# Kernel tuning notes

Measured on AMD Instinct MI355X. Metric: run time of the kernel, lower is better.

The kernel has to match this reference:

```python
import jax, jax.numpy as jnp
import numpy as np
from jax import lax

B, DIN, DOUT, DEPTH = 4096, 2048, 2048, 16


def setup_inputs() -> dict:
    key = jax.random.key(0)
    k1, k2, k3, k4 = jax.random.split(key, 4)
    return {
        "x": jax.random.normal(k1, (B, DIN), jnp.float32),
        "absolute_weights": jax.random.normal(k2, (DEPTH, DIN, DOUT), jnp.float32),
        "classical_weights": jax.random.normal(k3, (DIN, DOUT), jnp.float32),
        "classical_biases": jax.random.normal(k4, (DOUT,), jnp.float32),
    }


def _absolute_probs(W):
    # W: [depth, din, dout]; the torch code indexes W[d, j, g] with j over
    # output dims and g in {0,1,2} (3 gates per depth step).
    din = W.shape[1]
    dout = DOUT
    # angles per output j, flattened over (depth, gate): [dout, depth*3]
    ang = jnp.transpose(W[:, :dout, :3], (1, 0, 2)).reshape(dout, -1)
    s0 = jnp.ones((din,), W.dtype) / np.float32(np.sqrt(din))

    def step(s, a):
        # The dense "rotation" matrix built in torch is: diag=cos,
        # superdiag (wrapped) = -sin, subdiag (wrapped) = +sin, i.e.
        # (M s)[i] = cos*s[i] - sin*s[(i+1)%n] + sin*s[(i-1)%n].
        c, si = jnp.cos(a), jnp.sin(a)
        s_new = c * s - si * jnp.roll(s, -1) + si * jnp.roll(s, 1)
        return s_new, None

    def per_j(angs):
        s, _ = lax.scan(step, s0, angs)
        return jnp.abs(s[0]) ** 2

    return jax.vmap(per_j)(ang)  # [dout]


def reference(x, absolute_weights, classical_weights, classical_biases):
    classical = x @ classical_weights + classical_biases  # [B, dout]
    probs = _absolute_probs(absolute_weights)             # [dout], batch-independent
    return jnp.tanh(classical + probs[None, :])
```

## Files before the change

kernel.cpp:

```cpp
#include <hip/hip_runtime.h>
#include <math.h>

#define BATCH 4096
#define DIN   2048
#define DOUT  2048
#define DEPTH 16

typedef unsigned short u16;
typedef __attribute__((ext_vector_type(8))) short short8;
typedef __attribute__((ext_vector_type(4))) float f32x4;


__device__ static inline unsigned bf16_rn(float x) {
    unsigned u = __float_as_uint(x);
    return (u + 0x7FFFu + ((u >> 16) & 1u)) >> 16;
}

__device__ static inline float tanh_fast(float z) {
    float zc = fminf(fmaxf(z, -15.0f), 15.0f);
    float e = __builtin_amdgcn_exp2f(zc * 2.8853900817779268f);
    return (e - 1.0f) * __builtin_amdgcn_rcpf(e + 1.0f);
}

__device__ static inline void async16(u16* lds, const u16* g) {
    __builtin_amdgcn_global_load_lds(
        (const __attribute__((address_space(1))) void*)g,
        (__attribute__((address_space(3))) void*)lds, 16, 0, 0);
}

__global__ __launch_bounds__(256) void probs_kernel(const float* __restrict__ W,
                                                    float* __restrict__ probs) {
    int tid = threadIdx.x;
    int jl = tid >> 4, d = tid & 15;
    int j = blockIdx.x * 16 + jl;
    const float* p = W + (size_t)d * DIN * DOUT + (size_t)j * DOUT;
    float pr = cosf(p[0]) * cosf(p[1]) * cosf(p[2]);
#pragma unroll
    for (int off = 1; off < 16; off <<= 1) pr *= __shfl_xor(pr, off, 16);
    if (d == 0) probs[j] = pr * pr * (1.0f / (float)DIN);
}

__global__ __launch_bounds__(256) void convert_x_kernel(const float* __restrict__ x,
                                                        u16* __restrict__ xh,
                                                        u16* __restrict__ xl) {
    int i = (blockIdx.x * 256 + threadIdx.x) * 4;
    float4 v = *(const float4*)(x + i);
    ushort4 h, l;
    float vv[4] = {v.x, v.y, v.z, v.w};
    u16 hh[4], ll[4];
#pragma unroll
    for (int c = 0; c < 4; ++c) {
        unsigned hb = bf16_rn(vv[c]);
        hh[c] = (u16)hb;
        float r = vv[c] - __uint_as_float(hb << 16);
        ll[c] = (u16)bf16_rn(r);
    }
    h.x = hh[0]; h.y = hh[1]; h.z = hh[2]; h.w = hh[3];
    l.x = ll[0]; l.y = ll[1]; l.z = ll[2]; l.w = ll[3];
    *(ushort4*)(xh + i) = h;
    *(ushort4*)(xl + i) = l;
}

__global__ __launch_bounds__(256) void transpose_w_kernel(const float* __restrict__ W,
                                                          u16* __restrict__ wh,
                                                          u16* __restrict__ wl) {
    __shared__ float t[32][33];
    int n0 = blockIdx.x * 32, k0 = blockIdx.y * 32;
    int tx = threadIdx.x & 31, ty = threadIdx.x >> 5;
#pragma unroll
    for (int i = 0; i < 4; ++i)
        t[ty + i * 8][tx] = W[(size_t)(k0 + ty + i * 8) * DOUT + n0 + tx];
    __syncthreads();
#pragma unroll
    for (int i = 0; i < 4; ++i) {
        float v = t[tx][ty + i * 8];
        size_t o = (size_t)(n0 + ty + i * 8) * DIN + k0 + tx;
        unsigned hb = bf16_rn(v);
        wh[o] = (u16)hb;
        float r = v - __uint_as_float(hb << 16);
        wl[o] = (u16)bf16_rn(r);
    }
}

__global__ __launch_bounds__(256, 2) void gemm_mfma_kernel(
    const u16* __restrict__ xh, const u16* __restrict__ xl,
    const u16* __restrict__ wh, const u16* __restrict__ wl,
    const float* __restrict__ bias, const float* __restrict__ probs,
    float* __restrict__ C)
{
    __shared__ u16 sAh[4096];
    __shared__ u16 sAl[4096];
    __shared__ u16 sBh[4096];
    __shared__ u16 sBl[4096];

    const int tid = threadIdx.x;
    const int lane = tid & 63;
    const int wave = tid >> 6;
    const int bR = blockIdx.y * 128;
    const int bC = blockIdx.x * 128;

    const u16* gsrc = (wave == 0) ? xh + (size_t)bR * DIN
                    : (wave == 1) ? xl + (size_t)bR * DIN
                    : (wave == 2) ? wh + (size_t)bC * DIN
                                  : wl + (size_t)bC * DIN;
    u16* lbase = (wave == 0) ? sAh : (wave == 1) ? sAl : (wave == 2) ? sBh : sBl;

    int goff[8];
#pragma unroll
    for (int i = 0; i < 8; ++i) {
        int row = i * 16 + (lane >> 2);
        int lq = (lane & 3) ^ ((row >> 1) & 3);
        goff[i] = row * DIN + lq * 8;
    }

    const int wm = wave >> 1, wn = wave & 1;
    const int colL = lane & 15, quad = lane >> 4;

    int aoff[4], boff[4];
#pragma unroll
    for (int mt = 0; mt < 4; ++mt) {
        int r = wm * 64 + mt * 16 + colL;
        aoff[mt] = r * 32 + (quad ^ ((r >> 1) & 3)) * 8;
    }
#pragma unroll
    for (int nt = 0; nt < 4; ++nt) {
        int r = wn * 64 + nt * 16 + colL;
        boff[nt] = r * 32 + (quad ^ ((r >> 1) & 3)) * 8;
    }

    f32x4 acc[4][4];
#pragma unroll
    for (int mt = 0; mt < 4; ++mt)
#pragma unroll
        for (int nt = 0; nt < 4; ++nt) acc[mt][nt] = (f32x4){0.f, 0.f, 0.f, 0.f};

    for (int k0 = 0; k0 < DIN; k0 += 32) {
        __syncthreads();
#pragma unroll
        for (int i = 0; i < 8; ++i)
            async16(lbase + i * 512, gsrc + goff[i] + k0);
        __syncthreads();

        short8 ah[4], al[4], bh[4], bl[4];
#pragma unroll
        for (int mt = 0; mt < 4; ++mt) {
            ah[mt] = *(const short8*)&sAh[aoff[mt]];
            al[mt] = *(const short8*)&sAl[aoff[mt]];
        }
#pragma unroll
        for (int nt = 0; nt < 4; ++nt) {
            bh[nt] = *(const short8*)&sBh[boff[nt]];
            bl[nt] = *(const short8*)&sBl[boff[nt]];
        }

#pragma unroll
        for (int mt = 0; mt < 4; ++mt)
#pragma unroll
            for (int nt = 0; nt < 4; ++nt) {
                acc[mt][nt] = __builtin_amdgcn_mfma_f32_16x16x32_bf16(
                    ah[mt], bh[nt], acc[mt][nt], 0, 0, 0);
                acc[mt][nt] = __builtin_amdgcn_mfma_f32_16x16x32_bf16(
                    ah[mt], bl[nt], acc[mt][nt], 0, 0, 0);
                acc[mt][nt] = __builtin_amdgcn_mfma_f32_16x16x32_bf16(
                    al[mt], bh[nt], acc[mt][nt], 0, 0, 0);
            }
    }

    float bp[4];
#pragma unroll
    for (int nt = 0; nt < 4; ++nt) {
        int c = bC + wn * 64 + nt * 16 + colL;
        bp[nt] = bias[c] + probs[c];
    }
#pragma unroll
    for (int mt = 0; mt < 4; ++mt)
#pragma unroll
        for (int nt = 0; nt < 4; ++nt) {
            int c = bC + wn * 64 + nt * 16 + colL;
#pragma unroll
            for (int reg = 0; reg < 4; ++reg) {
                int r = bR + wm * 64 + mt * 16 + quad * 4 + reg;
                C[(size_t)r * DOUT + c] = tanh_fast(acc[mt][nt][reg] + bp[nt]);
            }
        }
}

__global__ __launch_bounds__(256) void gemm_tanh_kernel(
    const float* __restrict__ A, const float* __restrict__ Bw,
    const float* __restrict__ bias, const float* __restrict__ probs,
    float* __restrict__ C)
{
    __shared__ float As[16][128 + 4];
    __shared__ float Bs[16][128 + 4];
    const int tid = threadIdx.x;
    const int block_row = blockIdx.y * 128;
    const int block_col = blockIdx.x * 128;
    const int tr = (tid >> 4) << 3;
    const int tc = (tid & 15) << 3;
    const int a_row = tid >> 2;
    const int a_col = (tid & 3) << 2;
    const int b_row = tid >> 5;
    const int b_col = (tid & 31) << 2;
    const float* Aptr0 = A + (size_t)(block_row + a_row) * DIN + a_col;
    const float* Aptr1 = Aptr0 + (size_t)64 * DIN;
    const float* Bptr0 = Bw + (size_t)b_row * DOUT + block_col + b_col;
    const float* Bptr1 = Bptr0 + (size_t)8 * DOUT;
    float acc[8][8] = {};
    for (int k0 = 0; k0 < DIN; k0 += 16) {
        float4 a0 = *(const float4*)(Aptr0 + k0);
        float4 a1 = *(const float4*)(Aptr1 + k0);
        float4 b0 = *(const float4*)(Bptr0 + (size_t)k0 * DOUT);
        float4 b1 = *(const float4*)(Bptr1 + (size_t)k0 * DOUT);
        __syncthreads();
        As[a_col + 0][a_row] = a0.x;
        As[a_col + 1][a_row] = a0.y;
        As[a_col + 2][a_row] = a0.z;
        As[a_col + 3][a_row] = a0.w;
        As[a_col + 0][a_row + 64] = a1.x;
        As[a_col + 1][a_row + 64] = a1.y;
        As[a_col + 2][a_row + 64] = a1.z;
        As[a_col + 3][a_row + 64] = a1.w;
        *(float4*)&Bs[b_row][b_col]     = b0;
        *(float4*)&Bs[b_row + 8][b_col] = b1;
        __syncthreads();
#pragma unroll
        for (int kk = 0; kk < 16; ++kk) {
            float ar[8], br[8];
#pragma unroll
            for (int i = 0; i < 8; ++i) ar[i] = As[kk][tr + i];
#pragma unroll
            for (int i = 0; i < 8; ++i) br[i] = Bs[kk][tc + i];
#pragma unroll
            for (int i = 0; i < 8; ++i)
#pragma unroll
                for (int jj = 0; jj < 8; ++jj)
                    acc[i][jj] = fmaf(ar[i], br[jj], acc[i][jj]);
        }
    }
    float bp[8];
#pragma unroll
    for (int jj = 0; jj < 8; ++jj)
        bp[jj] = bias[block_col + tc + jj] + probs[block_col + tc + jj];
#pragma unroll
    for (int i = 0; i < 8; ++i) {
        float* crow = C + (size_t)(block_row + tr + i) * DOUT + block_col + tc;
#pragma unroll
        for (int jj = 0; jj < 8; ++jj)
            crow[jj] = tanh_fast(acc[i][jj] + bp[jj]);
    }
}

extern "C" void kernel_launch(void* const* d_in, const int* in_sizes, int n_in,
                              void* d_out, int out_size, void* d_ws, size_t ws_size,
                              hipStream_t stream) {
    const float* x  = (const float*)d_in[0];
    const float* W  = (const float*)d_in[1];
    const float* cw = (const float*)d_in[2];
    const float* cb = (const float*)d_in[3];
    float* out = (float*)d_out;

    const size_t PROBS_B = 8192;
    const size_t XSZ = (size_t)BATCH * DIN;
    const size_t WSZ = (size_t)DIN * DOUT;
    const size_t need = PROBS_B + 2 * XSZ * 2 + 2 * WSZ * 2;

    float* probs = (float*)d_ws;
    probs_kernel<<<DOUT / 16, 256, 0, stream>>>(W, probs);

    if (ws_size >= need) {
        u16* xh = (u16*)((char*)d_ws + PROBS_B);
        u16* xl = xh + XSZ;
        u16* wh = xl + XSZ;
        u16* wl = wh + WSZ;

        convert_x_kernel<<<XSZ / 4 / 256, 256, 0, stream>>>(x, xh, xl);
        transpose_w_kernel<<<dim3(DOUT / 32, DIN / 32), 256, 0, stream>>>(cw, wh, wl);

        dim3 grid(DOUT / 128, BATCH / 128);
        gemm_mfma_kernel<<<grid, 256, 0, stream>>>(xh, xl, wh, wl, cb, probs, out);
    } else {
        dim3 grid(DOUT / 128, BATCH / 128);
        gemm_tanh_kernel<<<grid, 256, 0, stream>>>(x, cw, cb, probs, out);
    }
}
```

Baseline: 432.6 us.

## Fuse preprocessing, probs and MFMA GEMM into one cooperative kernel with grid sync

Merges the probs, x split-conversion, weight transpose/split and MFMA GEMM kernels into a single cooperative launch of 512 blocks. Each block does a slice of the preprocessing, then all blocks meet at a grid-wide barrier before running the GEMM tile. The bias is folded into the probs vector ahead of time. This removes three kernel launches and the gaps between them, at the cost of a grid sync and a dependence on all 512 blocks being co-resident. It also drops the fp32 fallback path, so it needs enough workspace.

```diff
diff --git a/kernel.cpp b/kernel.cpp
--- a/kernel.cpp
+++ b/kernel.cpp
@@ -1,5 +1,8 @@
 #include <hip/hip_runtime.h>
+#include <hip/hip_cooperative_groups.h>
 #include <math.h>
+
+namespace cg = cooperative_groups;
 
 #define BATCH 4096
 #define DIN   2048
@@ -28,76 +31,87 @@
         (__attribute__((address_space(3))) void*)lds, 16, 0, 0);
 }
 
-__global__ __launch_bounds__(256) void probs_kernel(const float* __restrict__ W,
-                                                    float* __restrict__ probs) {
-    int tid = threadIdx.x;
-    int jl = tid >> 4, d = tid & 15;
-    int j = blockIdx.x * 16 + jl;
-    const float* p = W + (size_t)d * DIN * DOUT + (size_t)j * DOUT;
-    float pr = cosf(p[0]) * cosf(p[1]) * cosf(p[2]);
-#pragma unroll
-    for (int off = 1; off < 16; off <<= 1) pr *= __shfl_xor(pr, off, 16);
-    if (d == 0) probs[j] = pr * pr * (1.0f / (float)DIN);
-}
-
-__global__ __launch_bounds__(256) void convert_x_kernel(const float* __restrict__ x,
-                                                        u16* __restrict__ xh,
-                                                        u16* __restrict__ xl) {
-    int i = (blockIdx.x * 256 + threadIdx.x) * 4;
-    float4 v = *(const float4*)(x + i);
-    ushort4 h, l;
-    float vv[4] = {v.x, v.y, v.z, v.w};
-    u16 hh[4], ll[4];
-#pragma unroll
-    for (int c = 0; c < 4; ++c) {
-        unsigned hb = bf16_rn(vv[c]);
-        hh[c] = (u16)hb;
-        float r = vv[c] - __uint_as_float(hb << 16);
-        ll[c] = (u16)bf16_rn(r);
-    }
-    h.x = hh[0]; h.y = hh[1]; h.z = hh[2]; h.w = hh[3];
-    l.x = ll[0]; l.y = ll[1]; l.z = ll[2]; l.w = ll[3];
-    *(ushort4*)(xh + i) = h;
-    *(ushort4*)(xl + i) = l;
-}
-
-__global__ __launch_bounds__(256) void transpose_w_kernel(const float* __restrict__ W,
-                                                          u16* __restrict__ wh,
-                                                          u16* __restrict__ wl) {
-    __shared__ float t[32][33];
-    int n0 = blockIdx.x * 32, k0 = blockIdx.y * 32;
-    int tx = threadIdx.x & 31, ty = threadIdx.x >> 5;
-#pragma unroll
-    for (int i = 0; i < 4; ++i)
-        t[ty + i * 8][tx] = W[(size_t)(k0 + ty + i * 8) * DOUT + n0 + tx];
-    __syncthreads();
-#pragma unroll
-    for (int i = 0; i < 4; ++i) {
-        float v = t[tx][ty + i * 8];
-        size_t o = (size_t)(n0 + ty + i * 8) * DIN + k0 + tx;
-        unsigned hb = bf16_rn(v);
-        wh[o] = (u16)hb;
-        float r = v - __uint_as_float(hb << 16);
-        wl[o] = (u16)bf16_rn(r);
-    }
-}
-
-__global__ __launch_bounds__(256, 2) void gemm_mfma_kernel(
-    const u16* __restrict__ xh, const u16* __restrict__ xl,
-    const u16* __restrict__ wh, const u16* __restrict__ wl,
-    const float* __restrict__ bias, const float* __restrict__ probs,
+__global__ __launch_bounds__(256, 2) void fused_kernel(
+    const float* __restrict__ x,
+    const float* __restrict__ W,
+    const float* __restrict__ cw,
+    const float* __restrict__ cb,
+    u16* __restrict__ xh, u16* __restrict__ xl,
+    u16* __restrict__ wh, u16* __restrict__ wl,
+    float* __restrict__ bp,
     float* __restrict__ C)
 {
-    __shared__ u16 sAh[4096];
-    __shared__ u16 sAl[4096];
-    __shared__ u16 sBh[4096];
-    __shared__ u16 sBl[4096];
-
+    __shared__ u16 smem[16384];
     const int tid = threadIdx.x;
+    const int bid = blockIdx.x;
+
+#pragma unroll
+    for (int g = 0; g < 16; ++g) {
+        int i = (bid * 4096 + g * 256 + tid) * 4;
+        float4 v = *(const float4*)(x + i);
+        float vv[4] = {v.x, v.y, v.z, v.w};
+        u16 hh[4], ll[4];
+#pragma unroll
+        for (int c = 0; c < 4; ++c) {
+            unsigned hb = bf16_rn(vv[c]);
+            hh[c] = (u16)hb;
+            float r = vv[c] - __uint_as_float(hb << 16);
+            ll[c] = (u16)bf16_rn(r);
+        }
+        ushort4 h, l;
+        h.x = hh[0]; h.y = hh[1]; h.z = hh[2]; h.w = hh[3];
+        l.x = ll[0]; l.y = ll[1]; l.z = ll[2]; l.w = ll[3];
+        *(ushort4*)(xh + i) = h;
+        *(ushort4*)(xl + i) = l;
+    }
+
+    {
+        float* t = (float*)smem;
+        const int tx = tid & 31, ty = tid >> 5;
+#pragma unroll
+        for (int it = 0; it < 8; ++it) {
+            int tile = bid * 8 + it;
+            int n0 = (tile & 63) * 32;
+            int k0 = (tile >> 6) * 32;
+            __syncthreads();
+#pragma unroll
+            for (int r = 0; r < 4; ++r)
+                t[(ty + r * 8) * 33 + tx] =
+                    cw[(size_t)(k0 + ty + r * 8) * DOUT + n0 + tx];
+            __syncthreads();
+#pragma unroll
+            for (int r = 0; r < 4; ++r) {
+                float v = t[tx * 33 + ty + r * 8];
+                size_t o = (size_t)(n0 + ty + r * 8) * DIN + k0 + tx;
+                unsigned hb = bf16_rn(v);
+                wh[o] = (u16)hb;
+                float rr = v - __uint_as_float(hb << 16);
+                wl[o] = (u16)bf16_rn(rr);
+            }
+        }
+    }
+
+    if (bid < 128) {
+        int jl = tid >> 4, d = tid & 15;
+        int j = bid * 16 + jl;
+        const float* p = W + (size_t)d * DIN * DOUT + (size_t)j * DOUT;
+        float pr = cosf(p[0]) * cosf(p[1]) * cosf(p[2]);
+#pragma unroll
+        for (int off = 1; off < 16; off <<= 1) pr *= __shfl_xor(pr, off, 16);
+        if (d == 0) bp[j] = pr * pr * (1.0f / (float)DIN) + cb[j];
+    }
+
+    cg::this_grid().sync();
+
+    u16* sAh = smem;
+    u16* sAl = smem + 4096;
+    u16* sBh = smem + 8192;
+    u16* sBl = smem + 12288;
+
     const int lane = tid & 63;
     const int wave = tid >> 6;
-    const int bR = blockIdx.y * 128;
-    const int bC = blockIdx.x * 128;
+    const int bC = (bid & 15) * 128;
+    const int bR = (bid >> 4) * 128;
 
     const u16* gsrc = (wave == 0) ? xh + (size_t)bR * DIN
                     : (wave == 1) ? xl + (size_t)bR * DIN
@@ -166,12 +180,10 @@
             }
     }
 
-    float bp[4];
-#pragma unroll
-    for (int nt = 0; nt < 4; ++nt) {
-        int c = bC + wn * 64 + nt * 16 + colL;
-        bp[nt] = bias[c] + probs[c];
-    }
+    float bpv[4];
+#pragma unroll
+    for (int nt = 0; nt < 4; ++nt)
+        bpv[nt] = bp[bC + wn * 64 + nt * 16 + colL];
 #pragma unroll
     for (int mt = 0; mt < 4; ++mt)
 #pragma unroll
@@ -180,74 +192,9 @@
 #pragma unroll
             for (int reg = 0; reg < 4; ++reg) {
                 int r = bR + wm * 64 + mt * 16 + quad * 4 + reg;
-                C[(size_t)r * DOUT + c] = tanh_fast(acc[mt][nt][reg] + bp[nt]);
+                C[(size_t)r * DOUT + c] = tanh_fast(acc[mt][nt][reg] + bpv[nt]);
             }
         }
-}
-
-__global__ __launch_bounds__(256) void gemm_tanh_kernel(
-    const float* __restrict__ A, const float* __restrict__ Bw,
-    const float* __restrict__ bias, const float* __restrict__ probs,
-    float* __restrict__ C)
-{
-    __shared__ float As[16][128 + 4];
-    __shared__ float Bs[16][128 + 4];
-    const int tid = threadIdx.x;
-    const int block_row = blockIdx.y * 128;
-    const int block_col = blockIdx.x * 128;
-    const int tr = (tid >> 4) << 3;
-    const int tc = (tid & 15) << 3;
-    const int a_row = tid >> 2;
-    const int a_col = (tid & 3) << 2;
-    const int b_row = tid >> 5;
-    const int b_col = (tid & 31) << 2;
-    const float* Aptr0 = A + (size_t)(block_row + a_row) * DIN + a_col;
-    const float* Aptr1 = Aptr0 + (size_t)64 * DIN;
-    const float* Bptr0 = Bw + (size_t)b_row * DOUT + block_col + b_col;
-    const float* Bptr1 = Bptr0 + (size_t)8 * DOUT;
-    float acc[8][8] = {};
-    for (int k0 = 0; k0 < DIN; k0 += 16) {
-        float4 a0 = *(const float4*)(Aptr0 + k0);
-        float4 a1 = *(const float4*)(Aptr1 + k0);
-        float4 b0 = *(const float4*)(Bptr0 + (size_t)k0 * DOUT);
-        float4 b1 = *(const float4*)(Bptr1 + (size_t)k0 * DOUT);
-        __syncthreads();
-        As[a_col + 0][a_row] = a0.x;
-        As[a_col + 1][a_row] = a0.y;
-        As[a_col + 2][a_row] = a0.z;
-        As[a_col + 3][a_row] = a0.w;
-        As[a_col + 0][a_row + 64] = a1.x;
-        As[a_col + 1][a_row + 64] = a1.y;
-        As[a_col + 2][a_row + 64] = a1.z;
-        As[a_col + 3][a_row + 64] = a1.w;
-        *(float4*)&Bs[b_row][b_col]     = b0;
-        *(float4*)&Bs[b_row + 8][b_col] = b1;
-        __syncthreads();
-#pragma unroll
-        for (int kk = 0; kk < 16; ++kk) {
-            float ar[8], br[8];
-#pragma unroll
-            for (int i = 0; i < 8; ++i) ar[i] = As[kk][tr + i];
-#pragma unroll
-            for (int i = 0; i < 8; ++i) br[i] = Bs[kk][tc + i];
-#pragma unroll
-            for (int i = 0; i < 8; ++i)
-#pragma unroll
-                for (int jj = 0; jj < 8; ++jj)
-                    acc[i][jj] = fmaf(ar[i], br[jj], acc[i][jj]);
-        }
-    }
-    float bp[8];
-#pragma unroll
-    for (int jj = 0; jj < 8; ++jj)
-        bp[jj] = bias[block_col + tc + jj] + probs[block_col + tc + jj];
-#pragma unroll
-    for (int i = 0; i < 8; ++i) {
-        float* crow = C + (size_t)(block_row + tr + i) * DOUT + block_col + tc;
-#pragma unroll
-        for (int jj = 0; jj < 8; ++jj)
-            crow[jj] = tanh_fast(acc[i][jj] + bp[jj]);
-    }
 }
 
 extern "C" void kernel_launch(void* const* d_in, const int* in_sizes, int n_in,
@@ -262,24 +209,16 @@
     const size_t PROBS_B = 8192;
     const size_t XSZ = (size_t)BATCH * DIN;
     const size_t WSZ = (size_t)DIN * DOUT;
-    const size_t need = PROBS_B + 2 * XSZ * 2 + 2 * WSZ * 2;
-
-    float* probs = (float*)d_ws;
-    probs_kernel<<<DOUT / 16, 256, 0, stream>>>(W, probs);
-
-    if (ws_size >= need) {
-        u16* xh = (u16*)((char*)d_ws + PROBS_B);
-        u16* xl = xh + XSZ;
-        u16* wh = xl + XSZ;
-        u16* wl = wh + WSZ;
-
-        convert_x_kernel<<<XSZ / 4 / 256, 256, 0, stream>>>(x, xh, xl);
-        transpose_w_kernel<<<dim3(DOUT / 32, DIN / 32), 256, 0, stream>>>(cw, wh, wl);
-
-        dim3 grid(DOUT / 128, BATCH / 128);
-        gemm_mfma_kernel<<<grid, 256, 0, stream>>>(xh, xl, wh, wl, cb, probs, out);
-    } else {
-        dim3 grid(DOUT / 128, BATCH / 128);
-        gemm_tanh_kernel<<<grid, 256, 0, stream>>>(x, cw, cb, probs, out);
-    }
-}
+
+    float* bp = (float*)d_ws;
+    u16* xh = (u16*)((char*)d_ws + PROBS_B);
+    u16* xl = xh + XSZ;
+    u16* wh = xl + XSZ;
+    u16* wl = wh + WSZ;
+
+    void* args[] = {(void*)&x, (void*)&W, (void*)&cw, (void*)&cb,
+                    (void*)&xh, (void*)&xl, (void*)&wh, (void*)&wl,
+                    (void*)&bp, (void*)&out};
+    hipLaunchCooperativeKernel((void*)fused_kernel, dim3(512), dim3(256),
+                               args, 0, stream);
+}
```

Measured after the change: 497.0 us. 1.15x slower.
